# Optimization experiments

Hardware: AMD Instinct MI355X
Metric: run time of the kernel (lower is better)

The kernel has to match this reference:

```python
import jax, jax.numpy as jnp
import numpy as np

B, T, H = 8, 2048, 2048

def glorot(key, shape):
    return jax.random.uniform(key, shape, minval=-1.0, maxval=1.0) * jnp.sqrt(2 / sum(shape))

def setup_inputs() -> dict:
    key = jax.random.key(0)
    kx, kr, ka, kb = jax.random.split(key, 4)
    x_seq = jax.random.normal(kx, (B, T, H), dtype=jnp.float32)
    reset = jax.random.randint(kr, (B, T), 0, 2).astype(bool)
    a_mat = glorot(ka, (H, H))
    b_mat = glorot(kb, (H, H))
    return {"x_seq": x_seq, "reset": reset, "a_mat": a_mat, "b_mat": b_mat}

def reference(x_seq, reset, a_mat, b_mat):
    # Precompute B^T x_t for all timesteps in one big GEMM: (B^T x)_k = sum_h b[h,k] x[h]
    bx = jnp.einsum('hk,bth->btk', b_mat, x_seq)  # [B,T,H]
    bx_t = jnp.swapaxes(bx, 0, 1)                 # [T,B,H] time-major
    reset_t = jnp.swapaxes(reset, 0, 1)           # [T,B]

    def step(h, inp):
        bx_step, r = inp                          # [B,H], [B]
        h = jnp.where(r[:, None], 0.0, h)         # reset hidden state
        h = h @ a_mat.T + bx_step                 # A @ h per batch row
        return h, h

    h0 = jnp.zeros((B, H), dtype=x_seq.dtype)
    _, h_seq = jax.lax.scan(step, h0, (bx_t, reset_t))
    return jnp.swapaxes(h_seq, 0, 1)              # [B,T,H]
```

## Files before the change

kernel.cpp:

```cpp
#include <hip/hip_runtime.h>

#define Hn 2048
#define Bn 8
#define Tn 2048
#define Cn 16
#define NCn (Tn / Cn)
#define M2n (NCn * Bn)

using f32x4 = __attribute__((ext_vector_type(4))) float;
using u32x4 = __attribute__((ext_vector_type(4))) unsigned int;
using us4   = __attribute__((ext_vector_type(4))) unsigned short;
using bf8   = __attribute__((ext_vector_type(8))) short;
using f4    = __attribute__((ext_vector_type(4))) float;

#define GLOAD16(g, l) __builtin_amdgcn_global_load_lds(                      \
    (const __attribute__((address_space(1))) void*)(g),                      \
    (__attribute__((address_space(3))) void*)(l), 16, 0, 0)

__device__ __forceinline__ unsigned short f2bf(float f) {
    unsigned u = __builtin_bit_cast(unsigned, f);
    u = u + 0x7fffu + ((u >> 16) & 1u);
    return (unsigned short)(u >> 16);
}
__device__ __forceinline__ float bf2f(unsigned short h) {
    unsigned u = ((unsigned)h) << 16;
    return __builtin_bit_cast(float, u);
}
__device__ __forceinline__ void split2f(float v, unsigned short& a, unsigned short& b) {
    a = f2bf(v);
    b = f2bf(v - bf2f(a));
}

__global__ __launch_bounds__(256) void k_prep(const float* __restrict__ A,
                                              unsigned short* __restrict__ a1,
                                              unsigned short* __restrict__ a2,
                                              const float* __restrict__ Bm,
                                              unsigned short* __restrict__ b1,
                                              unsigned short* __restrict__ b2,
                                              const float* __restrict__ X,
                                              unsigned short* __restrict__ x1,
                                              unsigned short* __restrict__ x2,
                                              const unsigned int* __restrict__ rin,
                                              unsigned char* __restrict__ r8,
                                              int* __restrict__ cut,
                                              int* __restrict__ firstReset,
                                              int* __restrict__ anyUncut,
                                              int* __restrict__ perm,
                                              int* __restrict__ iperm,
                                              int* __restrict__ counts) {
    const int bid = blockIdx.x;
    if (bid < 4096) {
        size_t i = ((size_t)bid * 256 + threadIdx.x) * 4;
        f32x4 v = *(const f32x4*)&A[i];
        us4 h1, h2;
#pragma unroll
        for (int e = 0; e < 4; e++) {
            unsigned short p, r;
            split2f(v[e], p, r);
            h1[e] = p; h2[e] = r;
        }
        *(us4*)&a1[i] = h1; *(us4*)&a2[i] = h2;
        return;
    }
    if (bid < 5120) {
        __shared__ float tile[64][65];
        int t = bid - 4096;
        const int k0 = (t >> 5) * 64, n0 = (t & 31) * 64;
        const int c = threadIdx.x & 63, r4 = threadIdx.x >> 6;
#pragma unroll
        for (int i = 0; i < 16; i++) {
            int r = r4 * 16 + i;
            tile[r][c] = Bm[(size_t)(k0 + r) * Hn + n0 + c];
        }
        __syncthreads();
#pragma unroll
        for (int i = 0; i < 16; i++) {
            int r = r4 * 16 + i;
            float v = tile[c][r];
            unsigned short p, q;
            split2f(v, p, q);
            b1[(size_t)(n0 + r) * Hn + k0 + c] = p;
            b2[(size_t)(n0 + r) * Hn + k0 + c] = q;
        }
        return;
    }
    if (bid == 5120) {
        __shared__ int s_badInt, s_badFloat;
        __shared__ int hist[17], off[18], cur[17];
        if (threadIdx.x == 0) { s_badInt = 0; s_badFloat = 0; *anyUncut = 0; }
        if (threadIdx.x < 17) hist[threadIdx.x] = 0;
        __syncthreads();
        int badI = 0, badF = 0;
        for (int i = threadIdx.x; i < 4096; i += 256) {
            unsigned int v = rin[i];
            if (v > 1u) badI = 1;
            if (v != 0u && v != 0x3f800000u) badF = 1;
        }
        if (badI) atomicOr(&s_badInt, 1);
        if (badF) atomicOr(&s_badFloat, 1);
        __syncthreads();
        const int fmt = (!s_badInt) ? 0 : ((!s_badFloat) ? 1 : 2);
        const unsigned char* rb = (const unsigned char*)rin;
        const float* rf = (const float*)rin;
        for (int i = threadIdx.x; i < Bn * Tn; i += 256) {
            unsigned char v;
            if (fmt == 0)      v = (unsigned char)(rin[i] != 0u);
            else if (fmt == 1) v = (unsigned char)(rf[i] != 0.0f);
            else               v = (unsigned char)(rb[i] != 0);
            r8[i] = v;
        }
        __syncthreads();
        int anyU = 0;
        for (int m = threadIdx.x; m < M2n; m += 256) {
            int c = m / Bn, b = m % Bn;
            int fr = Cn;
            for (int j = 0; j < Cn; j++) {
                if (r8[b * Tn + c * Cn + j]) { fr = j; break; }
            }
            firstReset[m] = fr;
            int ct = (fr < Cn);
            cut[m] = ct;
            if (!ct && c < NCn - 1) anyU = 1;
            atomicAdd(&hist[fr], 1);
        }
        if (anyU) atomicOr(anyUncut, 1);
        __syncthreads();
        if (threadIdx.x == 0) {
            off[16] = 0;
            for (int v = 15; v >= 0; v--) off[v] = off[v + 1] + hist[v + 1];
            for (int v = 0; v < 17; v++) cur[v] = (v == 16) ? 0 : off[v];
            for (int j = 0; j < 16; j++) counts[j] = off[j];
        }
        __syncthreads();
        for (int m = threadIdx.x; m < M2n; m += 256) {
            int fr = firstReset[m];
            int pos = atomicAdd(&cur[fr], 1);
            perm[pos] = m;
            iperm[m] = pos;
        }
        return;
    }
    {
        size_t i = ((size_t)(bid - 5121) * 256 + threadIdx.x) * 4;
        f32x4 v = *(const f32x4*)&X[i];
        us4 h1, h2;
#pragma unroll
        for (int e = 0; e < 4; e++) {
            unsigned short p, r;
            split2f(v[e], p, r);
            h1[e] = p; h2[e] = r;
        }
        *(us4*)&x1[i] = h1; *(us4*)&x2[i] = h2;
    }
}

template<int PREX>
__global__ __launch_bounds__(512) void k_gemm_p1(const unsigned short* __restrict__ X0,
                                                 const unsigned short* __restrict__ X1,
                                                 const unsigned short* __restrict__ B0,
                                                 const unsigned short* __restrict__ B1,
                                                 const float* __restrict__ Xf,
                                                 float* __restrict__ Out,
                                                 unsigned short* __restrict__ S0,
                                                 unsigned short* __restrict__ S1) {
    constexpr int BM = 256, BN = 128, LW = 32;
    __shared__ unsigned short ldsA[2 * BM * LW];
    __shared__ unsigned short ldsB[2 * BN * LW];
    const int tid = threadIdx.x;
    const int lane = tid & 63;
    const int wv = tid >> 6;
    const int wm = wv >> 1, wn = wv & 1;
    const int n0 = blockIdx.x * BN;
    const int m0 = blockIdx.y * BM;

    f4 acc[4][4];
#pragma unroll
    for (int fm = 0; fm < 4; fm++)
#pragma unroll
        for (int fn = 0; fn < 4; fn++) acc[fm][fn] = (f4){0.f, 0.f, 0.f, 0.f};

    const unsigned short* gA[4];
    unsigned short* lA[4];
    const float* gX[2];
    unsigned short* lX[2];
    const unsigned short* gB[2];
    unsigned short* lB[2];
    if constexpr (PREX) {
#pragma unroll
        for (int q = 0; q < 4; q++) {
            int u = tid + q * 512;
            int sp = u >> 10, row = (u >> 2) & 255, slot = u & 3;
            int g = slot ^ ((row >> 1) & 3);
            gA[q] = (sp ? X1 : X0) + (size_t)(m0 + row) * Hn + g * 8;
            lA[q] = &ldsA[u * 8];
        }
    } else {
#pragma unroll
        for (int q = 0; q < 2; q++) {
            int u = tid + q * 512;
            int row = u >> 2, slot = u & 3;
            int s = slot ^ ((row >> 1) & 3);
            gX[q] = Xf + (size_t)(m0 + row) * Hn + slot * 8;
            lX[q] = &ldsA[row * LW + s * 8];
        }
    }
#pragma unroll
    for (int q = 0; q < 2; q++) {
        int u = tid + q * 512;
        int sp = u >> 9, row = (u >> 2) & 127, slot = u & 3;
        int g = slot ^ ((row >> 1) & 3);
        gB[q] = (sp ? B1 : B0) + (size_t)(n0 + row) * Hn + g * 8;
        lB[q] = &ldsB[u * 8];
    }
    const int sl = (lane >> 4) ^ ((lane >> 1) & 3);
    const int pa[3] = {0, 0, 1};
    const int pb[3] = {0, 1, 0};

    for (int k0 = 0; k0 < Hn; k0 += 32) {
        if constexpr (PREX) {
#pragma unroll
            for (int q = 0; q < 4; q++) {
                GLOAD16(gA[q], lA[q]);
                gA[q] += 32;
            }
        } else {
#pragma unroll
            for (int q = 0; q < 2; q++) {
                f32x4 va = *(const f32x4*)gX[q];
                f32x4 vb = *(const f32x4*)(gX[q] + 4);
                gX[q] += 32;
                us4 h1a, h2a, h1b, h2b;
#pragma unroll
                for (int e = 0; e < 4; e++) {
                    unsigned short p, r;
                    split2f(va[e], p, r); h1a[e] = p; h2a[e] = r;
                    split2f(vb[e], p, r); h1b[e] = p; h2b[e] = r;
                }
                *(us4*)lX[q] = h1a;
                *(us4*)(lX[q] + 4) = h1b;
                *(us4*)(lX[q] + BM * LW) = h2a;
                *(us4*)(lX[q] + BM * LW + 4) = h2b;
            }
        }
#pragma unroll
        for (int q = 0; q < 2; q++) {
            GLOAD16(gB[q], lB[q]);
            gB[q] += 32;
        }
        __syncthreads();

        bf8 af[2][4], bfr[2][4];
#pragma unroll
        for (int sp = 0; sp < 2; sp++)
#pragma unroll
            for (int f = 0; f < 4; f++)
                af[sp][f] = *(const bf8*)&ldsA[(sp * BM + wm * 64 + f * 16 + (lane & 15)) * LW + sl * 8];
#pragma unroll
        for (int sp = 0; sp < 2; sp++)
#pragma unroll
            for (int f = 0; f < 4; f++)
                bfr[sp][f] = *(const bf8*)&ldsB[(sp * BN + wn * 64 + f * 16 + (lane & 15)) * LW + sl * 8];

#pragma unroll
        for (int p = 0; p < 3; p++)
#pragma unroll
            for (int fm = 0; fm < 4; fm++)
#pragma unroll
                for (int fn = 0; fn < 4; fn++)
                    acc[fm][fn] = __builtin_amdgcn_mfma_f32_16x16x32_bf16(
                        af[pa[p]][fm], bfr[pb[p]][fn], acc[fm][fn], 0, 0, 0);
        __syncthreads();
    }

#pragma unroll
    for (int fm = 0; fm < 4; fm++)
#pragma unroll
        for (int r = 0; r < 4; r++) {
            int row = m0 + wm * 64 + fm * 16 + (lane >> 4) * 4 + r;
            int bb = row >> 11, t = row & 2047;
            int isC0 = ((t & 15) == 0);
            size_t ob = (size_t)row * Hn;
            size_t sb = (size_t)((t >> 4) * 8 + bb) * Hn;
#pragma unroll
            for (int fn = 0; fn < 4; fn++) {
                int n = n0 + wn * 64 + fn * 16 + (lane & 15);
                float v = acc[fm][fn][r];
                Out[ob + n] = v;
                if (isC0) {
                    unsigned short h1, h2;
                    split2f(v, h1, h2);
                    S0[sb + n] = h1; S1[sb + n] = h2;
                }
            }
        }
}

template<int PHASE>
__global__ __launch_bounds__(256) void k_gemm_s(const unsigned short* __restrict__ S0,
                                                const unsigned short* __restrict__ S1,
                                                const unsigned short* __restrict__ W0,
                                                const unsigned short* __restrict__ W1,
                                                float* __restrict__ Out,
                                                unsigned short* __restrict__ O0,
                                                unsigned short* __restrict__ O1,
                                                const unsigned char* __restrict__ r8v,
                                                const int* __restrict__ perm,
                                                const int* __restrict__ iperm,
                                                const int* __restrict__ counts,
                                                unsigned short* __restrict__ U0,
                                                unsigned short* __restrict__ U1,
                                                float* __restrict__ Hin,
                                                int j) {
    constexpr int BM = 64, BN = 64, BK = 64;
    constexpr int TSZ = 2 * BM * BK;
    constexpr int NT = Hn / BK;
    __shared__ unsigned short ldsA[2 * TSZ];
    __shared__ unsigned short ldsB[2 * TSZ];
    const int tid = threadIdx.x;
    const int lane = tid & 63;
    const int wv = tid >> 6;
    const int wm = wv >> 1, wn = wv & 1;
    const int n0 = blockIdx.x * BN;
    const int m0 = blockIdx.y * BM;

    int cnt = 0;
    if constexpr (PHASE == 4) {
        cnt = counts[j];
        if (m0 >= cnt) return;
    }

    f4 acc[2][2];
#pragma unroll
    for (int fm = 0; fm < 2; fm++)
#pragma unroll
        for (int fn = 0; fn < 2; fn++) acc[fm][fn] = (f4){0.f, 0.f, 0.f, 0.f};

    const unsigned short* gA[4];
    unsigned short* lA[4];
    const unsigned short* gB[4];
    unsigned short* lB[4];
#pragma unroll
    for (int q = 0; q < 4; q++) {
        int u = tid + q * 256;
        int sp = u >> 9, row = (u >> 3) & 63, s = u & 7;
        int g = s ^ (row & 7);
        gA[q] = (sp ? S1 : S0) + (size_t)(m0 + row) * Hn + g * 8;
        lA[q] = &ldsA[u * 8];
        gB[q] = (sp ? W1 : W0) + (size_t)(n0 + row) * Hn + g * 8;
        lB[q] = &ldsB[u * 8];
    }
    const int pa[3] = {0, 0, 1};
    const int pb[3] = {0, 1, 0};

#define STAGE_S(bsel)                                                        \
    {                                                                        \
        const int boff_ = (bsel) * TSZ;                                      \
        _Pragma("unroll")                                                    \
        for (int q = 0; q < 4; q++) {                                        \
            GLOAD16(gA[q], lA[q] + boff_);                                   \
            GLOAD16(gB[q], lB[q] + boff_);                                   \
            gA[q] += BK; gB[q] += BK;                                        \
        }                                                                    \
    }

    STAGE_S(0);
    STAGE_S(1);

    for (int t = 0; t < NT; t++) {
        if (t == NT - 1) { asm volatile("s_waitcnt vmcnt(0)" ::: "memory"); }
        else             { asm volatile("s_waitcnt vmcnt(8)" ::: "memory"); }
        __builtin_amdgcn_sched_barrier(0);
        __builtin_amdgcn_s_barrier();

        const unsigned short* curA = &ldsA[(t & 1) * TSZ];
        const unsigned short* curB = &ldsB[(t & 1) * TSZ];
        bf8 af[2][2][2], bfr[2][2][2];
#pragma unroll
        for (int h = 0; h < 2; h++) {
            const int slh = ((h * 4) + (lane >> 4)) ^ (lane & 7);
#pragma unroll
            for (int sp = 0; sp < 2; sp++)
#pragma unroll
                for (int f = 0; f < 2; f++) {
                    af[h][sp][f] = *(const bf8*)&curA[(sp * BM + wm * 32 + f * 16 + (lane & 15)) * BK + slh * 8];
                    bfr[h][sp][f] = *(const bf8*)&curB[(sp * BN + wn * 32 + f * 16 + (lane & 15)) * BK + slh * 8];
                }
        }
        asm volatile("s_waitcnt lgkmcnt(0)" ::: "memory");
        __builtin_amdgcn_sched_barrier(0);
        __builtin_amdgcn_s_barrier();

        if (t + 2 < NT) STAGE_S(t & 1);
        __builtin_amdgcn_sched_barrier(0);

        __builtin_amdgcn_s_setprio(1);
#pragma unroll
        for (int h = 0; h < 2; h++)
#pragma unroll
            for (int p = 0; p < 3; p++)
#pragma unroll
                for (int fm = 0; fm < 2; fm++)
#pragma unroll
                    for (int fn = 0; fn < 2; fn++)
                        acc[fm][fn] = __builtin_amdgcn_mfma_f32_16x16x32_bf16(
                            af[h][pa[p]][fm], bfr[h][pb[p]][fn], acc[fm][fn], 0, 0, 0);
        __builtin_amdgcn_s_setprio(0);
    }
#undef STAGE_S

    if constexpr (PHASE == 2 || PHASE == 3) {
#pragma unroll
        for (int fm = 0; fm < 2; fm++)
#pragma unroll
            for (int r = 0; r < 4; r++) {
                int m = m0 + wm * 32 + fm * 16 + (lane >> 4) * 4 + r;
                int cch = m >> 3, bb = m & 7;
                int t = cch * Cn + j;
                int rfl = r8v[bb * Tn + t];
                size_t ob = ((size_t)bb * Tn + t) * (size_t)Hn;
                size_t sb = (size_t)m * Hn;
                int carry = 0;
                size_t ub = 0, hb = 0;
                if constexpr (PHASE == 3) {
                    carry = (m < M2n - 8);
                    if (carry) {
                        ub = (size_t)iperm[m + 8] * Hn;
                        hb = (size_t)(m + 8) * Hn;
                    }
                }
#pragma unroll
                for (int fn = 0; fn < 2; fn++) {
                    int n = n0 + wn * 32 + fn * 16 + (lane & 15);
                    float v = (rfl ? 0.0f : acc[fm][fn][r]) + Out[ob + n];
                    Out[ob + n] = v;
                    unsigned short h1, h2;
                    split2f(v, h1, h2);
                    O0[sb + n] = h1; O1[sb + n] = h2;
                    if constexpr (PHASE == 3) {
                        if (carry) {
                            U0[ub + n] = h1; U1[ub + n] = h2;
                            Hin[hb + n] = v;
                        }
                        if (m < 8) {
                            size_t zb = (size_t)iperm[m] * Hn;
                            U0[zb + n] = 0; U1[zb + n] = 0;
                            Hin[(size_t)m * Hn + n] = 0.0f;
                        }
                    }
                }
            }
    } else {
#pragma unroll
        for (int fm = 0; fm < 2; fm++)
#pragma unroll
            for (int r = 0; r < 4; r++) {
                int s = m0 + wm * 32 + fm * 16 + (lane >> 4) * 4 + r;
                int alive = (s < cnt);
                int m = perm[s];
                int cch = m >> 3, bb = m & 7;
                int t = cch * Cn + j;
                size_t ob = ((size_t)bb * Tn + t) * (size_t)Hn;
                size_t sb = (size_t)s * Hn;
#pragma unroll
                for (int fn = 0; fn < 2; fn++) {
                    int n = n0 + wn * 32 + fn * 16 + (lane & 15);
                    if (alive) {
                        float val = acc[fm][fn][r];
                        unsigned short h1, h2;
                        split2f(val, h1, h2);
                        O0[sb + n] = h1; O1[sb + n] = h2;
                        Out[ob + n] += val;
                    }
                }
            }
    }
}

__global__ __launch_bounds__(1024) void k_fallback(float* __restrict__ Hin,
                                                   const float* __restrict__ A,
                                                   const int* __restrict__ cut,
                                                   const int* __restrict__ anyUncut,
                                                   unsigned short* __restrict__ u1,
                                                   unsigned short* __restrict__ u2,
                                                   const int* __restrict__ iperm) {
    if (*anyUncut == 0) return;
    __shared__ float v0[Hn];
    __shared__ float v1[Hn];
    for (int c = 1; c < NCn; c++) {
        for (int b = 0; b < Bn; b++) {
            if (cut[(c - 1) * Bn + b]) continue;
            for (int n = threadIdx.x; n < Hn; n += 1024)
                v0[n] = Hin[((size_t)(c - 1) * Bn + b) * Hn + n];
            __syncthreads();
            for (int s = 0; s < Cn; s++) {
                float* pin = (s & 1) ? v1 : v0;
                float* pout = (s & 1) ? v0 : v1;
                for (int n = threadIdx.x; n < Hn; n += 1024) {
                    float accv = 0.0f;
                    const float* Ar = &A[(size_t)n * Hn];
                    for (int k = 0; k < Hn; k++) accv += pin[k] * Ar[k];
                    pout[n] = accv;
                }
                __syncthreads();
            }
            float* pres = (Cn & 1) ? v1 : v0;
            int mrow = c * Bn + b;
            size_t dst = (size_t)mrow * Hn;
            size_t sdst = (size_t)iperm[mrow] * Hn;
            for (int n = threadIdx.x; n < Hn; n += 1024) {
                float nv = Hin[dst + n] + pres[n];
                Hin[dst + n] = nv;
                unsigned short h1, h2;
                split2f(nv, h1, h2);
                u1[sdst + n] = h1; u2[sdst + n] = h2;
            }
            __syncthreads();
        }
    }
}

extern "C" void kernel_launch(void* const* d_in, const int* in_sizes, int n_in,
                              void* d_out, int out_size, void* d_ws, size_t ws_size,
                              hipStream_t stream) {
    const float* x = (const float*)d_in[0];
    const unsigned int* rst = (const unsigned int*)d_in[1];
    const float* Am = (const float*)d_in[2];
    const float* Bm = (const float*)d_in[3];
    float* Out = (float*)d_out;
    char* ws = (char*)d_ws;

    unsigned char* r8 = (unsigned char*)ws;
    int* cut = (int*)(ws + 16384);
    int* firstReset = (int*)(ws + 20480);
    int* perm = (int*)(ws + 24576);
    int* iperm = (int*)(ws + 28672);
    int* counts = (int*)(ws + 32768);
    int* anyUncut = (int*)(ws + 32832);
    unsigned short* a1 = (unsigned short*)(ws + 65536);
    unsigned short* a2 = a1 + 4194304;
    unsigned short* b1 = a2 + 4194304;
    unsigned short* b2 = b1 + 4194304;
    unsigned short* sP1 = b2 + 4194304;
    unsigned short* sP2 = sP1 + 2097152;
    unsigned short* sQ1 = sP2 + 2097152;
    unsigned short* sQ2 = sQ1 + 2097152;
    unsigned short* uP1 = sQ2 + 2097152;
    unsigned short* uP2 = uP1 + 2097152;
    float* Hin = (float*)(uP2 + 2097152);
    unsigned short* x1 = (unsigned short*)(Hin + 2097152);
    unsigned short* x2 = x1 + 33554432;
    const size_t NEED_X = 201392128ull;
    const bool prex = (ws_size >= NEED_X);

    int prep_grid = prex ? (5121 + 32768) : 5121;
    k_prep<<<prep_grid, 256, 0, stream>>>(Am, a1, a2, Bm, b1, b2,
                                          x, x1, x2, rst, r8, cut, firstReset,
                                          anyUncut, perm, iperm, counts);

    if (prex) {
        k_gemm_p1<1><<<dim3(Hn / 128, (Bn * Tn) / 256), 512, 0, stream>>>(
            x1, x2, b1, b2, nullptr, Out, sP1, sP2);
    } else {
        k_gemm_p1<0><<<dim3(Hn / 128, (Bn * Tn) / 256), 512, 0, stream>>>(
            nullptr, nullptr, b1, b2, x, Out, sP1, sP2);
    }

    for (int j = 1; j < Cn; j++) {
        const unsigned short* i1 = (j & 1) ? sP1 : sQ1;
        const unsigned short* i2 = (j & 1) ? sP2 : sQ2;
        unsigned short* o1 = (j & 1) ? sQ1 : sP1;
        unsigned short* o2 = (j & 1) ? sQ2 : sP2;
        if (j < Cn - 1) {
            k_gemm_s<2><<<dim3(Hn / 64, M2n / 64), 256, 0, stream>>>(
                i1, i2, a1, a2, Out, o1, o2, r8, nullptr, nullptr, nullptr,
                nullptr, nullptr, nullptr, j);
        } else {
            k_gemm_s<3><<<dim3(Hn / 64, M2n / 64), 256, 0, stream>>>(
                i1, i2, a1, a2, Out, o1, o2, r8, nullptr, iperm, nullptr,
                uP1, uP2, Hin, j);
        }
    }

    k_fallback<<<1, 1024, 0, stream>>>(Hin, Am, cut, anyUncut, uP1, uP2, iperm);

    for (int j = 0; j < Cn; j++) {
        const unsigned short* i1 = (j == 0) ? uP1 : ((j & 1) ? sP1 : sQ1);
        const unsigned short* i2 = (j == 0) ? uP2 : ((j & 1) ? sP2 : sQ2);
        unsigned short* o1 = (j & 1) ? sQ1 : sP1;
        unsigned short* o2 = (j & 1) ? sQ2 : sP2;
        k_gemm_s<4><<<dim3(Hn / 64, M2n / 64), 256, 0, stream>>>(
            i1, i2, a1, a2, Out, o1, o2, nullptr, perm, nullptr, counts,
            nullptr, nullptr, nullptr, j);
    }
}
```

Measured before the change: 1.235 ms.

## Fuse per-step scan GEMM launches into one cooperative persistent kernel

Replaces the 30 separate k_gemm_s launches and the k_fallback launch with a single cooperative kernel that loops over phases and separates them with grid.sync(). The fallback sequential path now runs on block 0 with 256 threads inside phase 15. The aim is to remove per-launch overhead and the tail gaps between dependent GEMM steps. In exchange it adds grid-barrier cost, a slower single-block fallback when resets leave chunks uncut, and relies on 512 blocks fitting co-resident. If the cooperative launch fails, it falls back to per-phase launches.

```diff
diff --git a/kernel.cpp b/kernel.cpp
--- a/kernel.cpp
+++ b/kernel.cpp
@@ -1,4 +1,7 @@
 #include <hip/hip_runtime.h>
+#include <hip/hip_cooperative_groups.h>
+
+namespace cg = cooperative_groups;
 
 #define Hn 2048
 #define Bn 8
@@ -295,62 +298,129 @@
         }
 }
 
-template<int PHASE>
-__global__ __launch_bounds__(256) void k_gemm_s(const unsigned short* __restrict__ S0,
-                                                const unsigned short* __restrict__ S1,
-                                                const unsigned short* __restrict__ W0,
-                                                const unsigned short* __restrict__ W1,
-                                                float* __restrict__ Out,
-                                                unsigned short* __restrict__ O0,
-                                                unsigned short* __restrict__ O1,
-                                                const unsigned char* __restrict__ r8v,
-                                                const int* __restrict__ perm,
-                                                const int* __restrict__ iperm,
-                                                const int* __restrict__ counts,
-                                                unsigned short* __restrict__ U0,
-                                                unsigned short* __restrict__ U1,
-                                                float* __restrict__ Hin,
-                                                int j) {
+__global__ __launch_bounds__(256) void k_scan_all(const unsigned short* __restrict__ a1,
+                                                  const unsigned short* __restrict__ a2,
+                                                  unsigned short* __restrict__ sP1,
+                                                  unsigned short* __restrict__ sP2,
+                                                  unsigned short* __restrict__ sQ1,
+                                                  unsigned short* __restrict__ sQ2,
+                                                  unsigned short* __restrict__ uP1,
+                                                  unsigned short* __restrict__ uP2,
+                                                  float* __restrict__ Out,
+                                                  float* __restrict__ Hin,
+                                                  const unsigned char* __restrict__ r8v,
+                                                  const int* __restrict__ perm,
+                                                  const int* __restrict__ iperm,
+                                                  const int* __restrict__ counts,
+                                                  const int* __restrict__ cut,
+                                                  const int* __restrict__ anyUncut,
+                                                  const float* __restrict__ Am,
+                                                  int ph0, int ph1) {
     constexpr int BM = 64, BN = 64, BK = 64;
     constexpr int TSZ = 2 * BM * BK;
     constexpr int NT = Hn / BK;
     __shared__ unsigned short ldsA[2 * TSZ];
     __shared__ unsigned short ldsB[2 * TSZ];
+    cg::grid_group grid = cg::this_grid();
+
     const int tid = threadIdx.x;
     const int lane = tid & 63;
     const int wv = tid >> 6;
     const int wm = wv >> 1, wn = wv & 1;
-    const int n0 = blockIdx.x * BN;
-    const int m0 = blockIdx.y * BM;
-
-    int cnt = 0;
-    if constexpr (PHASE == 4) {
-        cnt = counts[j];
-        if (m0 >= cnt) return;
-    }
-
-    f4 acc[2][2];
-#pragma unroll
-    for (int fm = 0; fm < 2; fm++)
-#pragma unroll
-        for (int fn = 0; fn < 2; fn++) acc[fm][fn] = (f4){0.f, 0.f, 0.f, 0.f};
-
-    const unsigned short* gA[4];
+    const int bid = blockIdx.x;
+    const int bx = bid & 31;
+    const int by = bid >> 5;
+    const int n0 = bx * BN;
+    const int m0 = by * BM;
+    const int pa[3] = {0, 0, 1};
+    const int pb[3] = {0, 1, 0};
+
+    int su[4], srow[4], ssp[4];
     unsigned short* lA[4];
-    const unsigned short* gB[4];
     unsigned short* lB[4];
+    const unsigned short* gB0[4];
 #pragma unroll
     for (int q = 0; q < 4; q++) {
         int u = tid + q * 256;
-        int sp = u >> 9, row = (u >> 3) & 63, s = u & 7;
-        int g = s ^ (row & 7);
-        gA[q] = (sp ? S1 : S0) + (size_t)(m0 + row) * Hn + g * 8;
+        ssp[q] = u >> 9;
+        srow[q] = (u >> 3) & 63;
+        int s = u & 7;
+        su[q] = (s ^ (srow[q] & 7)) * 8;
         lA[q] = &ldsA[u * 8];
-        gB[q] = (sp ? W1 : W0) + (size_t)(n0 + row) * Hn + g * 8;
         lB[q] = &ldsB[u * 8];
-    }
-    const int pa[3] = {0, 0, 1};
-    const int pb[3] = {0, 1, 0};
+        gB0[q] = (ssp[q] ? a2 : a1) + (size_t)(n0 + srow[q]) * Hn + su[q];
+    }
+
+    for (int ph = ph0; ph < ph1; ph++) {
+        if (ph == 15) {
+            if (bid == 0 && *anyUncut != 0) {
+                float* v0 = (float*)ldsA;
+                float* v1 = (float*)ldsB;
+                for (int c = 1; c < NCn; c++) {
+                    for (int b = 0; b < Bn; b++) {
+                        if (cut[(c - 1) * Bn + b]) continue;
+                        for (int n = tid; n < Hn; n += 256)
+                            v0[n] = Hin[((size_t)(c - 1) * Bn + b) * Hn + n];
+                        __syncthreads();
+                        for (int s = 0; s < Cn; s++) {
+                            float* pin = (s & 1) ? v1 : v0;
+                            float* pout = (s & 1) ? v0 : v1;
+                            for (int n = tid; n < Hn; n += 256) {
+                                float accv = 0.0f;
+                                const float* Ar = &Am[(size_t)n * Hn];
+                                for (int k = 0; k < Hn; k++) accv += pin[k] * Ar[k];
+                                pout[n] = accv;
+                            }
+                            __syncthreads();
+                        }
+                        float* pres = (Cn & 1) ? v1 : v0;
+                        int mrow = c * Bn + b;
+                        size_t dst = (size_t)mrow * Hn;
+                        size_t sdst = (size_t)iperm[mrow] * Hn;
+                        for (int n = tid; n < Hn; n += 256) {
+                            float nv = Hin[dst + n] + pres[n];
+                            Hin[dst + n] = nv;
+                            unsigned short h1, h2;
+                            split2f(nv, h1, h2);
+                            uP1[sdst + n] = h1; uP2[sdst + n] = h2;
+                        }
+                        __syncthreads();
+                    }
+                }
+            }
+        } else {
+            const int isScan = (ph < 15);
+            const int j = isScan ? (ph + 1) : (ph - 16);
+            const unsigned short *i1, *i2;
+            unsigned short *o1, *o2;
+            if (isScan) {
+                i1 = (j & 1) ? sP1 : sQ1;  i2 = (j & 1) ? sP2 : sQ2;
+            } else {
+                i1 = (j == 0) ? uP1 : ((j & 1) ? sP1 : sQ1);
+                i2 = (j == 0) ? uP2 : ((j & 1) ? sP2 : sQ2);
+            }
+            o1 = (j & 1) ? sQ1 : sP1;  o2 = (j & 1) ? sQ2 : sP2;
+
+            int cnt = 0;
+            int active = 1;
+            if (!isScan) {
+                cnt = counts[j];
+                active = (m0 < cnt);
+            }
+            if (active) {
+                f4 acc[2][2];
+#pragma unroll
+                for (int fm = 0; fm < 2; fm++)
+#pragma unroll
+                    for (int fn = 0; fn < 2; fn++) acc[fm][fn] = (f4){0.f, 0.f, 0.f, 0.f};
+
+                const unsigned short* gA[4];
+                const unsigned short* gB[4];
+#pragma unroll
+                for (int q = 0; q < 4; q++) {
+                    gA[q] = (ssp[q] ? i2 : i1) + (size_t)(m0 + srow[q]) * Hn + su[q];
+                    gB[q] = gB0[q];
+                }
 
 #define STAGE_S(bsel)                                                        \
     {                                                                        \
@@ -362,159 +432,124 @@
             gA[q] += BK; gB[q] += BK;                                        \
         }                                                                    \
     }
-
-    STAGE_S(0);
-    STAGE_S(1);
-
-    for (int t = 0; t < NT; t++) {
-        if (t == NT - 1) { asm volatile("s_waitcnt vmcnt(0)" ::: "memory"); }
-        else             { asm volatile("s_waitcnt vmcnt(8)" ::: "memory"); }
-        __builtin_amdgcn_sched_barrier(0);
-        __builtin_amdgcn_s_barrier();
-
-        const unsigned short* curA = &ldsA[(t & 1) * TSZ];
-        const unsigned short* curB = &ldsB[(t & 1) * TSZ];
-        bf8 af[2][2][2], bfr[2][2][2];
-#pragma unroll
-        for (int h = 0; h < 2; h++) {
-            const int slh = ((h * 4) + (lane >> 4)) ^ (lane & 7);
-#pragma unroll
-            for (int sp = 0; sp < 2; sp++)
-#pragma unroll
-                for (int f = 0; f < 2; f++) {
-                    af[h][sp][f] = *(const bf8*)&curA[(sp * BM + wm * 32 + f * 16 + (lane & 15)) * BK + slh * 8];
-                    bfr[h][sp][f] = *(const bf8*)&curB[(sp * BN + wn * 32 + f * 16 + (lane & 15)) * BK + slh * 8];
+                STAGE_S(0);
+                STAGE_S(1);
+
+                for (int t = 0; t < NT; t++) {
+                    if (t == NT - 1) { asm volatile("s_waitcnt vmcnt(0)" ::: "memory"); }
+                    else             { asm volatile("s_waitcnt vmcnt(8)" ::: "memory"); }
+                    __builtin_amdgcn_sched_barrier(0);
+                    __builtin_amdgcn_s_barrier();
+
+                    const unsigned short* curA = &ldsA[(t & 1) * TSZ];
+                    const unsigned short* curB = &ldsB[(t & 1) * TSZ];
+                    bf8 af[2][2][2], bfr[2][2][2];
+#pragma unroll
+                    for (int h = 0; h < 2; h++) {
+                        const int slh = ((h * 4) + (lane >> 4)) ^ (lane & 7);
+#pragma unroll
+                        for (int sp = 0; sp < 2; sp++)
+#pragma unroll
+                            for (int f = 0; f < 2; f++) {
+                                af[h][sp][f] = *(const bf8*)&curA[(sp * BM + wm * 32 + f * 16 + (lane & 15)) * BK + slh * 8];
+                                bfr[h][sp][f] = *(const bf8*)&curB[(sp * BN + wn * 32 + f * 16 + (lane & 15)) * BK + slh * 8];
+                            }
+                    }
+                    asm volatile("s_waitcnt lgkmcnt(0)" ::: "memory");
+                    __builtin_amdgcn_sched_barrier(0);
+                    __builtin_amdgcn_s_barrier();
+
+                    if (t + 2 < NT) STAGE_S(t & 1);
+                    __builtin_amdgcn_sched_barrier(0);
+
+                    __builtin_amdgcn_s_setprio(1);
+#pragma unroll
+                    for (int h = 0; h < 2; h++)
+#pragma unroll
+                        for (int p = 0; p < 3; p++)
+#pragma unroll
+                            for (int fm = 0; fm < 2; fm++)
+#pragma unroll
+                                for (int fn = 0; fn < 2; fn++)
+                                    acc[fm][fn] = __builtin_amdgcn_mfma_f32_16x16x32_bf16(
+                                        af[h][pa[p]][fm], bfr[h][pb[p]][fn], acc[fm][fn], 0, 0, 0);
+                    __builtin_amdgcn_s_setprio(0);
                 }
-        }
-        asm volatile("s_waitcnt lgkmcnt(0)" ::: "memory");
-        __builtin_amdgcn_sched_barrier(0);
-        __builtin_amdgcn_s_barrier();
-
-        if (t + 2 < NT) STAGE_S(t & 1);
-        __builtin_amdgcn_sched_barrier(0);
-
-        __builtin_amdgcn_s_setprio(1);
-#pragma unroll
-        for (int h = 0; h < 2; h++)
-#pragma unroll
-            for (int p = 0; p < 3; p++)
-#pragma unroll
-                for (int fm = 0; fm < 2; fm++)
-#pragma unroll
-                    for (int fn = 0; fn < 2; fn++)
-                        acc[fm][fn] = __builtin_amdgcn_mfma_f32_16x16x32_bf16(
-                            af[h][pa[p]][fm], bfr[h][pb[p]][fn], acc[fm][fn], 0, 0, 0);
-        __builtin_amdgcn_s_setprio(0);
-    }
 #undef STAGE_S
 
-    if constexpr (PHASE == 2 || PHASE == 3) {
-#pragma unroll
-        for (int fm = 0; fm < 2; fm++)
-#pragma unroll
-            for (int r = 0; r < 4; r++) {
-                int m = m0 + wm * 32 + fm * 16 + (lane >> 4) * 4 + r;
-                int cch = m >> 3, bb = m & 7;
-                int t = cch * Cn + j;
-                int rfl = r8v[bb * Tn + t];
-                size_t ob = ((size_t)bb * Tn + t) * (size_t)Hn;
-                size_t sb = (size_t)m * Hn;
-                int carry = 0;
-                size_t ub = 0, hb = 0;
-                if constexpr (PHASE == 3) {
-                    carry = (m < M2n - 8);
-                    if (carry) {
-                        ub = (size_t)iperm[m + 8] * Hn;
-                        hb = (size_t)(m + 8) * Hn;
-                    }
+                if (isScan) {
+                    const int doCarry = (j == Cn - 1);
+#pragma unroll
+                    for (int fm = 0; fm < 2; fm++)
+#pragma unroll
+                        for (int r = 0; r < 4; r++) {
+                            int m = m0 + wm * 32 + fm * 16 + (lane >> 4) * 4 + r;
+                            int cch = m >> 3, bb = m & 7;
+                            int t = cch * Cn + j;
+                            int rfl = r8v[bb * Tn + t];
+                            size_t ob = ((size_t)bb * Tn + t) * (size_t)Hn;
+                            size_t sb = (size_t)m * Hn;
+                            int carry = 0;
+                            size_t ub = 0, hb = 0;
+                            if (doCarry) {
+                                carry = (m < M2n - 8);
+                                if (carry) {
+                                    ub = (size_t)iperm[m + 8] * Hn;
+                                    hb = (size_t)(m + 8) * Hn;
+                                }
+                            }
+#pragma unroll
+                            for (int fn = 0; fn < 2; fn++) {
+                                int n = n0 + wn * 32 + fn * 16 + (lane & 15);
+                                float v = (rfl ? 0.0f : acc[fm][fn][r]) + Out[ob + n];
+                                Out[ob + n] = v;
+                                unsigned short h1, h2;
+                                split2f(v, h1, h2);
+                                O0_write:
+                                o1[sb + n] = h1; o2[sb + n] = h2;
+                                if (doCarry) {
+                                    if (carry) {
+                                        uP1[ub + n] = h1; uP2[ub + n] = h2;
+                                        Hin[hb + n] = v;
+                                    }
+                                    if (m < 8) {
+                                        size_t zb = (size_t)iperm[m] * Hn;
+                                        uP1[zb + n] = 0; uP2[zb + n] = 0;
+                                        Hin[(size_t)m * Hn + n] = 0.0f;
+                                    }
+                                }
+                            }
+                        }
+                } else {
+#pragma unroll
+                    for (int fm = 0; fm < 2; fm++)
+#pragma unroll
+                        for (int r = 0; r < 4; r++) {
+                            int s = m0 + wm * 32 + fm * 16 + (lane >> 4) * 4 + r;
+                            int alive = (s < cnt);
+                            int m = perm[s];
+                            int cch = m >> 3, bb = m & 7;
+                            int t = cch * Cn + j;
+                            size_t ob = ((size_t)bb * Tn + t) * (size_t)Hn;
+                            size_t sb = (size_t)s * Hn;
+#pragma unroll
+                            for (int fn = 0; fn < 2; fn++) {
+                                int n = n0 + wn * 32 + fn * 16 + (lane & 15);
+                                if (alive) {
+                                    float val = acc[fm][fn][r];
+                                    unsigned short h1, h2;
+                                    split2f(val, h1, h2);
+                                    o1[sb + n] = h1; o2[sb + n] = h2;
+                                    Out[ob + n] += val;
+                                }
+                            }
+                        }
                 }
-#pragma unroll
-                for (int fn = 0; fn < 2; fn++) {
-                    int n = n0 + wn * 32 + fn * 16 + (lane & 15);
-                    float v = (rfl ? 0.0f : acc[fm][fn][r]) + Out[ob + n];
-                    Out[ob + n] = v;
-                    unsigned short h1, h2;
-                    split2f(v, h1, h2);
-                    O0[sb + n] = h1; O1[sb + n] = h2;
-                    if constexpr (PHASE == 3) {
-                        if (carry) {
-                            U0[ub + n] = h1; U1[ub + n] = h2;
-                            Hin[hb + n] = v;
-                        }
-                        if (m < 8) {
-                            size_t zb = (size_t)iperm[m] * Hn;
-                            U0[zb + n] = 0; U1[zb + n] = 0;
-                            Hin[(size_t)m * Hn + n] = 0.0f;
-                        }
-                    }
-                }
-            }
-    } else {
-#pragma unroll
-        for (int fm = 0; fm < 2; fm++)
-#pragma unroll
-            for (int r = 0; r < 4; r++) {
-                int s = m0 + wm * 32 + fm * 16 + (lane >> 4) * 4 + r;
-                int alive = (s < cnt);
-                int m = perm[s];
-                int cch = m >> 3, bb = m & 7;
-                int t = cch * Cn + j;
-                size_t ob = ((size_t)bb * Tn + t) * (size_t)Hn;
-                size_t sb = (size_t)s * Hn;
-#pragma unroll
-                for (int fn = 0; fn < 2; fn++) {
-                    int n = n0 + wn * 32 + fn * 16 + (lane & 15);
-                    if (alive) {
-                        float val = acc[fm][fn][r];
-                        unsigned short h1, h2;
-                        split2f(val, h1, h2);
-                        O0[sb + n] = h1; O1[sb + n] = h2;
-                        Out[ob + n] += val;
-                    }
-                }
-            }
-    }
-}
-
-__global__ __launch_bounds__(1024) void k_fallback(float* __restrict__ Hin,
-                                                   const float* __restrict__ A,
-                                                   const int* __restrict__ cut,
-                                                   const int* __restrict__ anyUncut,
-                                                   unsigned short* __restrict__ u1,
-                                                   unsigned short* __restrict__ u2,
-                                                   const int* __restrict__ iperm) {
-    if (*anyUncut == 0) return;
-    __shared__ float v0[Hn];
-    __shared__ float v1[Hn];
-    for (int c = 1; c < NCn; c++) {
-        for (int b = 0; b < Bn; b++) {
-            if (cut[(c - 1) * Bn + b]) continue;
-            for (int n = threadIdx.x; n < Hn; n += 1024)
-                v0[n] = Hin[((size_t)(c - 1) * Bn + b) * Hn + n];
-            __syncthreads();
-            for (int s = 0; s < Cn; s++) {
-                float* pin = (s & 1) ? v1 : v0;
-                float* pout = (s & 1) ? v0 : v1;
-                for (int n = threadIdx.x; n < Hn; n += 1024) {
-                    float accv = 0.0f;
-                    const float* Ar = &A[(size_t)n * Hn];
-                    for (int k = 0; k < Hn; k++) accv += pin[k] * Ar[k];
-                    pout[n] = accv;
-                }
-                __syncthreads();
-            }
-            float* pres = (Cn & 1) ? v1 : v0;
-            int mrow = c * Bn + b;
-            size_t dst = (size_t)mrow * Hn;
-            size_t sdst = (size_t)iperm[mrow] * Hn;
-            for (int n = threadIdx.x; n < Hn; n += 1024) {
-                float nv = Hin[dst + n] + pres[n];
-                Hin[dst + n] = nv;
-                unsigned short h1, h2;
-                split2f(nv, h1, h2);
-                u1[sdst + n] = h1; u2[sdst + n] = h2;
-            }
-            __syncthreads();
+            }
+        }
+        if (ph + 1 < ph1) {
+            __threadfence();
+            grid.sync();
         }
     }
 }
@@ -565,31 +600,22 @@
             nullptr, nullptr, b1, b2, x, Out, sP1, sP2);
     }
 
-    for (int j = 1; j < Cn; j++) {
-        const unsigned short* i1 = (j & 1) ? sP1 : sQ1;
-        const unsigned short* i2 = (j & 1) ? sP2 : sQ2;
-        unsigned short* o1 = (j & 1) ? sQ1 : sP1;
-        unsigned short* o2 = (j & 1) ? sQ2 : sP2;
-        if (j < Cn - 1) {
-            k_gemm_s<2><<<dim3(Hn / 64, M2n / 64), 256, 0, stream>>>(
-                i1, i2, a1, a2, Out, o1, o2, r8, nullptr, nullptr, nullptr,
-                nullptr, nullptr, nullptr, j);
-        } else {
-            k_gemm_s<3><<<dim3(Hn / 64, M2n / 64), 256, 0, stream>>>(
-                i1, i2, a1, a2, Out, o1, o2, r8, nullptr, iperm, nullptr,
-                uP1, uP2, Hin, j);
-        }
-    }
-
-    k_fallback<<<1, 1024, 0, stream>>>(Hin, Am, cut, anyUncut, uP1, uP2, iperm);
-
-    for (int j = 0; j < Cn; j++) {
-        const unsigned short* i1 = (j == 0) ? uP1 : ((j & 1) ? sP1 : sQ1);
-        const unsigned short* i2 = (j == 0) ? uP2 : ((j & 1) ? sP2 : sQ2);
-        unsigned short* o1 = (j & 1) ? sQ1 : sP1;
-        unsigned short* o2 = (j & 1) ? sQ2 : sP2;
-        k_gemm_s<4><<<dim3(Hn / 64, M2n / 64), 256, 0, stream>>>(
-            i1, i2, a1, a2, Out, o1, o2, nullptr, perm, nullptr, counts,
-            nullptr, nullptr, nullptr, j);
+    int ph0 = 0, ph1 = 32;
+    void* args[] = {(void*)&a1, (void*)&a2, (void*)&sP1, (void*)&sP2,
+                    (void*)&sQ1, (void*)&sQ2, (void*)&uP1, (void*)&uP2,
+                    (void*)&Out, (void*)&Hin, (void*)&r8, (void*)&perm,
+                    (void*)&iperm, (void*)&counts, (void*)&cut,
+                    (void*)&anyUncut, (void*)&Am, (void*)&ph0, (void*)&ph1};
+    hipError_t e = hipLaunchCooperativeKernel((void*)k_scan_all,
+                                              dim3(512), dim3(256),
+                                              args, 0, stream);
+    if (e != hipSuccess) {
+        (void)hipGetLastError();
+        for (int p = 0; p < 32; p++) {
+            k_scan_all<<<512, 256, 0, stream>>>(a1, a2, sP1, sP2, sQ1, sQ2,
+                                                uP1, uP2, Out, Hin, r8, perm,
+                                                iperm, counts, cut, anyUncut,
+                                                Am, p, p + 1);
+        }
     }
 }
```

Result: slower. 4.332 ms (+250.7%).

## Load GEMM A fragments directly from global memory, bypassing LDS staging

Applied to the files above, without the earlier changes.

Drops the LDS double-buffer for the A (state) operand in the bf16 split GEMM kernel. Each wave now reads its A MFMA fragments straight from global memory into registers, while only the B (weight) tiles keep the async global-to-LDS prefetch, with the vmcnt threshold adjusted to match. The goal is to halve LDS footprint and LDS traffic per k-step. The cost is that global load latency for A sits directly in front of the MFMAs with no prefetch. A fragments are also fetched redundantly by the two waves that share a row block, and the per-lane reads are less coalesced.

```diff
diff --git a/kernel.cpp b/kernel.cpp
--- a/kernel.cpp
+++ b/kernel.cpp
@@ -312,9 +312,8 @@
                                                 float* __restrict__ Hin,
                                                 int j) {
     constexpr int BM = 64, BN = 64, BK = 64;
-    constexpr int TSZ = 2 * BM * BK;
+    constexpr int TSZ = 2 * BN * BK;
     constexpr int NT = Hn / BK;
-    __shared__ unsigned short ldsA[2 * TSZ];
     __shared__ unsigned short ldsB[2 * TSZ];
     const int tid = threadIdx.x;
     const int lane = tid & 63;
@@ -335,8 +334,6 @@
 #pragma unroll
         for (int fn = 0; fn < 2; fn++) acc[fm][fn] = (f4){0.f, 0.f, 0.f, 0.f};
 
-    const unsigned short* gA[4];
-    unsigned short* lA[4];
     const unsigned short* gB[4];
     unsigned short* lB[4];
 #pragma unroll
@@ -344,35 +341,42 @@
         int u = tid + q * 256;
         int sp = u >> 9, row = (u >> 3) & 63, s = u & 7;
         int g = s ^ (row & 7);
-        gA[q] = (sp ? S1 : S0) + (size_t)(m0 + row) * Hn + g * 8;
-        lA[q] = &ldsA[u * 8];
         gB[q] = (sp ? W1 : W0) + (size_t)(n0 + row) * Hn + g * 8;
         lB[q] = &ldsB[u * 8];
     }
+    const unsigned short* gAf[2][2][2];
+#pragma unroll
+    for (int h = 0; h < 2; h++)
+#pragma unroll
+        for (int sp = 0; sp < 2; sp++)
+#pragma unroll
+            for (int f = 0; f < 2; f++)
+                gAf[h][sp][f] = (sp ? S1 : S0)
+                    + (size_t)(m0 + wm * 32 + f * 16 + (lane & 15)) * Hn
+                    + h * 32 + (lane >> 4) * 8;
+
     const int pa[3] = {0, 0, 1};
     const int pb[3] = {0, 1, 0};
 
-#define STAGE_S(bsel)                                                        \
+#define STAGE_B(bsel)                                                        \
     {                                                                        \
         const int boff_ = (bsel) * TSZ;                                      \
         _Pragma("unroll")                                                    \
         for (int q = 0; q < 4; q++) {                                        \
-            GLOAD16(gA[q], lA[q] + boff_);                                   \
             GLOAD16(gB[q], lB[q] + boff_);                                   \
-            gA[q] += BK; gB[q] += BK;                                        \
+            gB[q] += BK;                                                     \
         }                                                                    \
     }
 
-    STAGE_S(0);
-    STAGE_S(1);
+    STAGE_B(0);
+    STAGE_B(1);
 
     for (int t = 0; t < NT; t++) {
         if (t == NT - 1) { asm volatile("s_waitcnt vmcnt(0)" ::: "memory"); }
-        else             { asm volatile("s_waitcnt vmcnt(8)" ::: "memory"); }
+        else             { asm volatile("s_waitcnt vmcnt(4)" ::: "memory"); }
         __builtin_amdgcn_sched_barrier(0);
         __builtin_amdgcn_s_barrier();
 
-        const unsigned short* curA = &ldsA[(t & 1) * TSZ];
         const unsigned short* curB = &ldsB[(t & 1) * TSZ];
         bf8 af[2][2][2], bfr[2][2][2];
 #pragma unroll
@@ -381,16 +385,23 @@
 #pragma unroll
             for (int sp = 0; sp < 2; sp++)
 #pragma unroll
+                for (int f = 0; f < 2; f++)
+                    bfr[h][sp][f] = *(const bf8*)&curB[(sp * BN + wn * 32 + f * 16 + (lane & 15)) * BK + slh * 8];
+        }
+#pragma unroll
+        for (int h = 0; h < 2; h++)
+#pragma unroll
+            for (int sp = 0; sp < 2; sp++)
+#pragma unroll
                 for (int f = 0; f < 2; f++) {
-                    af[h][sp][f] = *(const bf8*)&curA[(sp * BM + wm * 32 + f * 16 + (lane & 15)) * BK + slh * 8];
-                    bfr[h][sp][f] = *(const bf8*)&curB[(sp * BN + wn * 32 + f * 16 + (lane & 15)) * BK + slh * 8];
+                    af[h][sp][f] = *(const bf8*)gAf[h][sp][f];
+                    gAf[h][sp][f] += BK;
                 }
-        }
         asm volatile("s_waitcnt lgkmcnt(0)" ::: "memory");
         __builtin_amdgcn_sched_barrier(0);
         __builtin_amdgcn_s_barrier();
 
-        if (t + 2 < NT) STAGE_S(t & 1);
+        if (t + 2 < NT) STAGE_B(t & 1);
         __builtin_amdgcn_sched_barrier(0);
 
         __builtin_amdgcn_s_setprio(1);
@@ -406,7 +417,7 @@
                             af[h][pa[p]][fm], bfr[h][pb[p]][fn], acc[fm][fn], 0, 0, 0);
         __builtin_amdgcn_s_setprio(0);
     }
-#undef STAGE_S
+#undef STAGE_B
 
     if constexpr (PHASE == 2 || PHASE == 3) {
 #pragma unroll
```

Result: slower. 2.046 ms (+65.6%).
